# Kernel tuning notes

Measured on AMD Instinct MI355X. Metric: run time of the kernel, lower is better.

Reference implementation:

```python
import jax, jax.numpy as jnp
import numpy as np

N = 50000          # nodes
DEG = 8            # per-node in/out degree
E = N * DEG        # fwd edges (rev = reversed fwd)
H = 128            # hidden_dim
T = 4              # towers
F = H // T         # per-tower F_in (divide_input=True)
FO = H // T        # per-tower F_out
L = 2              # num_layers
IN_DIM = 128
OUT_DIM = 32
AVG_LOG = float(np.log(DEG + 1.0))  # avg of log(deg+1) from deg histogram (all deg==8)
BN_EPS = 1e-5
STD_EPS = 1e-5


def setup_inputs() -> dict:
    key = jax.random.key(0)
    ks = jax.random.split(key, 10)
    x = jax.random.normal(ks[0], (N, IN_DIM), jnp.float32)
    # every node appears exactly DEG times as dst and as src -> deg histogram delta at 8
    dst = jnp.repeat(jnp.arange(N, dtype=jnp.int32), DEG)
    src = jax.random.permutation(ks[1], dst)
    edge_fwd = jnp.stack([src, dst])  # [2, E]

    def rn(k, shape):
        return jax.random.normal(k, shape, jnp.float32) * 0.05

    return dict(
        x=x,
        W_in=rn(ks[2], (IN_DIM, H)), b_in=jnp.zeros((H,), jnp.float32),
        # [layer, relation(fwd/rev), tower, ...]
        pre_W=rn(ks[3], (L, 2, T, 2 * F, F)), pre_b=jnp.zeros((L, 2, T, F), jnp.float32),
        post_W=rn(ks[4], (L, 2, T, 13 * F, FO)), post_b=jnp.zeros((L, 2, T, FO), jnp.float32),
        lin_W=rn(ks[5], (L, 2, H, H)), lin_b=jnp.zeros((L, 2, H), jnp.float32),
        bn_gamma=jnp.ones((L, H), jnp.float32), bn_beta=jnp.zeros((L, H), jnp.float32),
        mlp_W1=rn(ks[6], (H, H)), mlp_b1=jnp.zeros((H,), jnp.float32),
        mlp_W2=rn(ks[7], (H, OUT_DIM)), mlp_b2=jnp.zeros((OUT_DIM,), jnp.float32),
        edge_fwd=edge_fwd,
    )


def _pna(x, src, dst, pre_W, pre_b, post_W, post_b, lin_W, lin_b):
    """One PNAConv (divide_input=True, pre/post_layers=1, no edge attr)."""
    xt = x.reshape(N, T, F)                                   # [N,T,F]
    # message: cat([x_i (dst), x_j (src)]) -> per-tower pre-MLP
    h = jnp.concatenate([xt[dst], xt[src]], axis=-1)          # [E,T,2F]
    m = jnp.einsum('etf,tfg->etg', h, pre_W) + pre_b          # [E,T,F]
    # multi-aggregator scatter reduce over destination nodes
    deg = jax.ops.segment_sum(jnp.ones((m.shape[0],), x.dtype), dst, N)
    degc = jnp.maximum(deg, 1.0)
    inv = (1.0 / degc)[:, None, None]
    mean = jax.ops.segment_sum(m, dst, N) * inv
    mean2 = jax.ops.segment_sum(m * m, dst, N) * inv
    std = jnp.sqrt(jax.nn.relu(mean2 - mean * mean) + STD_EPS)
    mn = jax.ops.segment_min(m, dst, N)
    mx = jax.ops.segment_max(m, dst, N)
    agg = jnp.concatenate([mean, mn, mx, std], axis=-1)       # [N,T,4F]
    # degree scalers: amplification, attenuation, identity
    ld = jnp.log(degc + 1.0)[:, None, None]
    agg = jnp.concatenate([agg * (ld / AVG_LOG), agg * (AVG_LOG / ld), agg], axis=-1)  # [N,T,12F]
    out = jnp.concatenate([xt, agg], axis=-1)                 # [N,T,13F]
    out = jnp.einsum('ntf,tfg->ntg', out, post_W) + post_b    # [N,T,FO]
    out = out.reshape(N, T * FO)
    return out @ lin_W + lin_b                                # [N,H]


def _bn(x, g, b):
    mu = x.mean(0)
    var = x.var(0)  # biased, as torch BatchNorm normalization
    return g * (x - mu) * jax.lax.rsqrt(var + BN_EPS) + b


def reference(x, W_in, b_in, pre_W, pre_b, post_W, post_b, lin_W, lin_b,
              bn_gamma, bn_beta, mlp_W1, mlp_b1, mlp_W2, mlp_b2, edge_fwd):
    src, dst = edge_fwd[0], edge_fwd[1]
    h = jax.nn.relu(x @ W_in + b_in)
    for l in range(L):
        # HeteroConv sum of fwd relation and rev relation (reversed edges)
        y = (_pna(h, src, dst, pre_W[l, 0], pre_b[l, 0], post_W[l, 0], post_b[l, 0], lin_W[l, 0], lin_b[l, 0])
             + _pna(h, dst, src, pre_W[l, 1], pre_b[l, 1], post_W[l, 1], post_b[l, 1], lin_W[l, 1], lin_b[l, 1]))
        h = jax.nn.relu(_bn(y, bn_gamma[l], bn_beta[l]))
        # dropout omitted (deterministic reference / eval mode)
    return jax.nn.relu(h @ mlp_W1 + mlp_b1) @ mlp_W2 + mlp_b2
```

## Files before the change

kernel.cpp:

```cpp
#include <hip/hip_runtime.h>
#include <hip/hip_fp16.h>
#include <cstddef>
#include <cstdint>

#define NN 50000
#define DEG 8
#define EE (NN*DEG)
#define RT_CNT 3125
#define KSTEPS 36
#define W8L 18432
#define MPAD 136

typedef __attribute__((ext_vector_type(8))) short short8;
typedef __attribute__((ext_vector_type(4))) float f32x4;

union Pack8 { __half h[8]; __half2 h2[4]; uint4 u; };
union Pack4 { __half h[4]; uint2 u; };

__global__ void k_build_nbr(const int* __restrict__ ef, int* __restrict__ cnt,
                            int* __restrict__ fwd_nbr, int* __restrict__ rev_nbr) {
    int e = blockIdx.x * blockDim.x + threadIdx.x;
    if (e >= EE) return;
    int s = ef[e], d = ef[EE + e];
    int p = atomicAdd(&cnt[d], 1);
    fwd_nbr[d * DEG + p] = s;
    int q = atomicAdd(&cnt[NN + s], 1);
    rev_nbr[s * DEG + q] = d;
}

__global__ __launch_bounds__(256) void k_wprep(
    const float* __restrict__ post_W, const float* __restrict__ pre_W,
    const float* __restrict__ pre_b, const float* __restrict__ post_b,
    const float* __restrict__ lin_W, const float* __restrict__ lin_b,
    __half* __restrict__ Wcp, float* __restrict__ Qw, float* __restrict__ bc) {
    __shared__ float Pf[160 * 33];
    __shared__ float Wl[32 * 128];
    __shared__ float Wt[32 * 32];
    __shared__ float Ps[32 * 32];
    __shared__ float Q[32 * 32];
    __shared__ float T3s[32];
    int tid = threadIdx.x;
    int m4 = blockIdx.x;
    int l = m4 >> 3, r = (m4 >> 2) & 1, tw = m4 & 3;
    const float* PW = post_W + (size_t)m4 * 416 * 32;
    for (int i = tid; i < 160 * 32; i += 256) {
        int row = i >> 5, g = i & 31;
        float v;
        if (row < 32) v = PW[row * 32 + g];
        else {
            int rr = row - 32;
            v = PW[(32 + rr) * 32 + g] + PW[(160 + rr) * 32 + g] + PW[(288 + rr) * 32 + g];
        }
        Pf[row * 33 + g] = v;
    }
    for (int i = tid; i < 1024; i += 256) Wt[i] = pre_W[(size_t)m4 * 2048 + i];
    for (int i = tid; i < 4096; i += 256)
        Wl[i] = lin_W[(size_t)(l * 2 + r) * 16384 + tw * 32 * 128 + i];
    __syncthreads();
    for (int i = tid; i < 1024; i += 256) {
        int g = i >> 5, j = i & 31;
        Ps[i] = Pf[(32 + g) * 33 + j] + Pf[(64 + g) * 33 + j] + Pf[(96 + g) * 33 + j];
    }
    __syncthreads();
    for (int i = tid; i < 1024; i += 256) {
        int f = i >> 5, j = i & 31;
        float acc = Pf[f * 33 + j];
#pragma unroll
        for (int g = 0; g < 32; g++) acc += Wt[f * 32 + g] * Ps[g * 32 + j];
        Q[i] = acc;
    }
    if (tid < 32) {
        int j = tid;
        float v = post_b[m4 * 32 + j];
#pragma unroll
        for (int g = 0; g < 32; g++) v += pre_b[m4 * 32 + g] * Ps[g * 32 + j];
        T3s[j] = v;
    }
    __syncthreads();
    for (int u = tid; u < 2048; u += 256) {
        int lane = u & 63, t = (u >> 6) & 7, s = u >> 9;
        int quad = lane >> 4, nl = lane & 15;
        int n = t * 16 + nl;
        Pack8 pk;
#pragma unroll
        for (int e = 0; e < 8; e++) {
            int f = quad * 8 + e;
            const float* Pr = &Pf[((s + 1) * 32 + f) * 33];
            float acc = 0.f;
#pragma unroll
            for (int j = 0; j < 32; j++) acc += Pr[j] * Wl[j * 128 + n];
            pk.h[e] = __float2half(acc);
        }
        int ks = 4 + r * 16 + tw * 4 + s;
        *(uint4*)&Wcp[((size_t)l * W8L + (t * KSTEPS + ks) * 64 + lane) * 8] = pk.u;
    }
    for (int i = tid; i < 4096; i += 256) {
        int f = i >> 7, n = i & 127;
        float acc = 0.f;
#pragma unroll
        for (int j = 0; j < 32; j++) acc += Q[f * 32 + j] * Wl[j * 128 + n];
        atomicAdd(&Qw[(size_t)l * 16384 + (tw * 32 + f) * 128 + n], acc);
    }
    if (tid < 128) {
        float v = 0.f;
#pragma unroll
        for (int j = 0; j < 32; j++) v += T3s[j] * Wl[j * 128 + tid];
        atomicAdd(&bc[l * 128 + tid], v);
        if ((m4 & 7) == 0)
            atomicAdd(&bc[l * 128 + tid],
                      lin_b[(2 * l) * 128 + tid] + lin_b[(2 * l + 1) * 128 + tid]);
    }
}

__global__ void k_pack_xt(const float* __restrict__ Qw, __half* __restrict__ Wcp) {
    int gid = blockIdx.x * blockDim.x + threadIdx.x;
    if (gid >= 2 * 4 * 8 * 64) return;
    int lane = gid & 63, t = (gid >> 6) & 7, ks = (gid >> 9) & 3, l = gid >> 11;
    int quad = lane >> 4;
    int n = t * 16 + (lane & 15);
    Pack8 pk;
#pragma unroll
    for (int e = 0; e < 8; e++)
        pk.h[e] = __float2half(Qw[(size_t)l * 16384 + (ks * 32 + quad * 8 + e) * 128 + n]);
    *(uint4*)&Wcp[((size_t)l * W8L + (t * KSTEPS + ks) * 64 + lane) * 8] = pk.u;
}

__global__ void k_pack_b(const float* __restrict__ W, int K, int N,
                         __half* __restrict__ dst) {
    int gid = blockIdx.x * blockDim.x + threadIdx.x;
    int total = (K >> 5) * (N >> 4) * 64;
    if (gid >= total) return;
    int lane = gid & 63;
    int ks = (gid >> 6) % (K >> 5);
    int t = (gid >> 6) / (K >> 5);
    int quad = lane >> 4, nl = lane & 15;
    int n = t * 16 + nl;
    Pack8 pk;
#pragma unroll
    for (int e = 0; e < 8; e++)
        pk.h[e] = __float2half(W[(size_t)(ks * 32 + quad * 8 + e) * N + n]);
    *(uint4*)&dst[(size_t)gid * 8] = pk.u;
}

__global__ __launch_bounds__(256) void k_in_mfma(
    const float* __restrict__ X, const __half* __restrict__ Wp,
    const float* __restrict__ b, float* __restrict__ H) {
    __shared__ __half Sh[4][16 * MPAD];
    int tid = threadIdx.x, wave = tid >> 6, lane = tid & 63;
    int rt = blockIdx.x * 4 + wave;
    if (rt >= RT_CNT) rt = RT_CNT - 1;
    __half* T = Sh[wave];
    const float4* X4 = (const float4*)X + (size_t)rt * 16 * 32;
#pragma unroll
    for (int i = 0; i < 8; i++) {
        int idx = i * 64 + lane;
        int row = idx >> 5, col4 = idx & 31;
        float4 v = X4[idx];
        Pack4 p4;
        p4.h[0] = __float2half(v.x); p4.h[1] = __float2half(v.y);
        p4.h[2] = __float2half(v.z); p4.h[3] = __float2half(v.w);
        *(uint2*)&T[row * MPAD + col4 * 4] = p4.u;
    }
    int mm = lane & 15, quad = lane >> 4;
    short8 a[4];
#pragma unroll
    for (int ks = 0; ks < 4; ks++)
        a[ks] = *(const short8*)&T[mm * MPAD + ks * 32 + quad * 8];
    const short8* Bb = (const short8*)Wp + lane;
    f32x4 acc[8];
#pragma unroll
    for (int t = 0; t < 8; t++) acc[t] = (f32x4){0.f, 0.f, 0.f, 0.f};
#pragma unroll
    for (int ks = 0; ks < 4; ks++)
#pragma unroll
        for (int t = 0; t < 8; t++)
            acc[t] = __builtin_amdgcn_mfma_f32_16x16x32_f16(
                a[ks], Bb[(t * 4 + ks) * 64], acc[t], 0, 0, 0);
#pragma unroll
    for (int t = 0; t < 8; t++) {
        int n = t * 16 + mm;
        float bias = b[n];
#pragma unroll
        for (int r = 0; r < 4; r++) {
            int node = rt * 16 + quad * 4 + r;
            H[(size_t)node * 128 + n] = fmaxf(acc[t][r] + bias, 0.f);
        }
    }
}

template<int BN>
__global__ __launch_bounds__(256) void k_preB(
    const float* __restrict__ Xin, const float* __restrict__ scale,
    const float* __restrict__ shift, float* __restrict__ hout,
    const float* __restrict__ pre_W, int layer, __half* __restrict__ Bplanes) {
    __shared__ float Wb[2 * 4 * 32 * 32];
    __shared__ float Xs[16 * 128];
    int tid = threadIdx.x;
    for (int i = tid; i < 8192; i += 256) {
        int g = i & 31, f = (i >> 5) & 31, t = (i >> 10) & 3, r = i >> 12;
        Wb[i] = pre_W[((((layer * 2 + r) * 4 + t) * 64) + 32 + f) * 32 + g];
    }
    int r = tid >> 7, c = tid & 127, t = c >> 5, g = c & 31;
    const float* wp = &Wb[((r * 4 + t) * 32) * 32 + g];
    int base = blockIdx.x * 16;
    for (int i = tid; i < 16 * 128; i += 256) {
        int col = i & 127;
        size_t gi = (size_t)(base + (i >> 7)) * 128 + col;
        float v = Xin[gi];
        if (BN) {
            v = fmaxf(scale[col] * v + shift[col], 0.f);
            hout[gi] = v;
        }
        Xs[i] = v;
    }
    __syncthreads();
    for (int n = 0; n < 16; n++) {
        float acc = 0.f;
#pragma unroll
        for (int f = 0; f < 32; f++) acc += Xs[n * 128 + t * 32 + f] * wp[f * 32];
        Bplanes[(size_t)r * NN * 128 + (size_t)(base + n) * 128 + c] = __float2half(acc);
    }
}

__global__ __launch_bounds__(256, 4) void k_agg_gemm(
    const float* __restrict__ hbuf, const __half* __restrict__ Bplanes,
    const int* __restrict__ fwd_nbr, const int* __restrict__ rev_nbr,
    const __half* __restrict__ Wcp, const float* __restrict__ bc,
    float* __restrict__ Y, float* __restrict__ bnsum, float* __restrict__ bnsum2) {
    __shared__ __half Spack[KSTEPS * 64 * 8];
    __shared__ float bnred[256];
    int tid = threadIdx.x;
    int blk = blockIdx.x;
    bnred[tid] = 0.f;
    int lane = tid & 63, wv = tid >> 6;
    int s = lane >> 4, f16 = lane & 15;
    int tw = f16 >> 2, quad = f16 & 3;
    int m = wv * 4 + s;
    int d = blk * 16 + m;
    {
        const int4* nf = (const int4*)&fwd_nbr[d * 8];
        const int4* nr = (const int4*)&rev_nbr[d * 8];
        int4 a0 = nf[0], a1 = nf[1], b0v = nr[0], b1v = nr[1];
        int idx0[8] = {a0.x, a0.y, a0.z, a0.w, a1.x, a1.y, a1.z, a1.w};
        int idx1[8] = {b0v.x, b0v.y, b0v.z, b0v.w, b1v.x, b1v.y, b1v.z, b1v.w};
        int fo = f16 * 8;
        Pack8 r0[8], r1[8];
        const __half* Bp1 = Bplanes + (size_t)NN * 128;
#pragma unroll
        for (int k = 0; k < 8; k++)
            r0[k].u = *(const uint4*)&Bplanes[(size_t)idx0[k] * 128 + fo];
#pragma unroll
        for (int k = 0; k < 8; k++)
            r1[k].u = *(const uint4*)&Bp1[(size_t)idx1[k] * 128 + fo];
        const float* Hp = &hbuf[(size_t)(blk * 16 + f16) * 128 + wv * 32 + s * 8];
        float4 xv0 = *(const float4*)Hp;
        float4 xv1 = *(const float4*)(Hp + 4);
        int pos = 16 * quad + (m ^ quad ^ ((tw & 1) << 2));
#pragma unroll
        for (int rel = 0; rel < 2; rel++) {
            Pack8* rr = rel ? r1 : r0;
            float sS[8], qS[8], mnS[8], mxS[8];
#pragma unroll
            for (int j = 0; j < 8; j++) {
                sS[j] = 0.f; qS[j] = 0.f; mnS[j] = 1e30f; mxS[j] = -1e30f;
            }
#pragma unroll
            for (int k = 0; k < 8; k++) {
#pragma unroll
                for (int j2 = 0; j2 < 4; j2++) {
                    __half2 h = rr[k].h2[j2];
                    float a = __half2float(__low2half(h));
                    float b = __half2float(__high2half(h));
                    int j0 = 2 * j2, j1 = j0 + 1;
                    sS[j0] += a; qS[j0] += a * a;
                    mnS[j0] = fminf(mnS[j0], a); mxS[j0] = fmaxf(mxS[j0], a);
                    sS[j1] += b; qS[j1] += b * b;
                    mnS[j1] = fminf(mnS[j1], b); mxS[j1] = fmaxf(mxS[j1], b);
                }
            }
            Pack8 mean, stdv, mnp, mxp;
#pragma unroll
            for (int j = 0; j < 8; j++) {
                float Bm = sS[j] * 0.125f;
                mean.h[j] = __float2half(Bm);
                stdv.h[j] = __float2half(
                    sqrtf(fmaxf(qS[j] * 0.125f - Bm * Bm, 0.f) + 1e-5f));
                mnp.h[j] = __float2half(mnS[j]);
                mxp.h[j] = __float2half(mxS[j]);
            }
            int ksb = 4 + rel * 16 + tw * 4;
            *(uint4*)&Spack[((size_t)(ksb + 0) * 64 + pos) * 8] = mean.u;
            *(uint4*)&Spack[((size_t)(ksb + 1) * 64 + pos) * 8] = mnp.u;
            *(uint4*)&Spack[((size_t)(ksb + 2) * 64 + pos) * 8] = mxp.u;
            *(uint4*)&Spack[((size_t)(ksb + 3) * 64 + pos) * 8] = stdv.u;
        }
        int posx = 16 * s + (f16 ^ s ^ ((wv & 1) << 2));
        Pack8 pk;
        pk.h[0] = __float2half(xv0.x); pk.h[1] = __float2half(xv0.y);
        pk.h[2] = __float2half(xv0.z); pk.h[3] = __float2half(xv0.w);
        pk.h[4] = __float2half(xv1.x); pk.h[5] = __float2half(xv1.y);
        pk.h[6] = __float2half(xv1.z); pk.h[7] = __float2half(xv1.w);
        *(uint4*)&Spack[((size_t)wv * 64 + posx) * 8] = pk.u;
    }
    __syncthreads();
    int mB = lane & 15, qB = lane >> 4;
    int t0 = wv * 2;
    const short8* Bb = (const short8*)Wcp + lane;
    f32x4 acc0 = (f32x4){0.f, 0.f, 0.f, 0.f};
    f32x4 acc1 = (f32x4){0.f, 0.f, 0.f, 0.f};
    short8 p0[6], p1[6];
#pragma unroll
    for (int dd = 0; dd < 6; dd++) {
        p0[dd] = Bb[((size_t)t0 * KSTEPS + dd) * 64];
        p1[dd] = Bb[((size_t)(t0 + 1) * KSTEPS + dd) * 64];
    }
#pragma unroll
    for (int ks = 0; ks < KSTEPS; ks++) {
        int twk = (ks < 4) ? ks : (((ks - 4) >> 2) & 3);
        int pos = 16 * qB + (mB ^ qB ^ ((twk & 1) << 2));
        short8 a = *(const short8*)&Spack[((size_t)ks * 64 + pos) * 8];
        acc0 = __builtin_amdgcn_mfma_f32_16x16x32_f16(a, p0[ks % 6], acc0, 0, 0, 0);
        acc1 = __builtin_amdgcn_mfma_f32_16x16x32_f16(a, p1[ks % 6], acc1, 0, 0, 0);
        if (ks + 6 < KSTEPS) {
            p0[ks % 6] = Bb[((size_t)t0 * KSTEPS + ks + 6) * 64];
            p1[ks % 6] = Bb[((size_t)(t0 + 1) * KSTEPS + ks + 6) * 64];
        }
    }
    int nl = lane & 15, qd = lane >> 4;
#pragma unroll
    for (int tt = 0; tt < 2; tt++) {
        f32x4 acc = tt ? acc1 : acc0;
        int n = (t0 + tt) * 16 + nl;
        float bias = bc[n];
        float ls = 0.f, ls2 = 0.f;
#pragma unroll
        for (int r = 0; r < 4; r++) {
            float v = acc[r] + bias;
            int node = blk * 16 + qd * 4 + r;
            Y[(size_t)node * 128 + n] = v;
            ls += v; ls2 += v * v;
        }
        ls += __shfl_xor(ls, 16); ls += __shfl_xor(ls, 32);
        ls2 += __shfl_xor(ls2, 16); ls2 += __shfl_xor(ls2, 32);
        if (qd == 0) { bnred[n] += ls; bnred[128 + n] += ls2; }
    }
    __syncthreads();
    if (tid < 128) {
        atomicAdd(&bnsum[tid], bnred[tid]);
        atomicAdd(&bnsum2[tid], bnred[128 + tid]);
    }
}

__global__ void k_bn_final(const float* __restrict__ bnsum, const float* __restrict__ bnsum2,
                           const float* __restrict__ gamma, const float* __restrict__ beta,
                           int layer, float* __restrict__ scale, float* __restrict__ shift) {
    int c = threadIdx.x;
    float mu = bnsum[c] * (1.f / NN);
    float var = bnsum2[c] * (1.f / NN) - mu * mu;
    float sc = gamma[layer * 128 + c] * rsqrtf(var + 1e-5f);
    scale[c] = sc;
    shift[c] = beta[layer * 128 + c] - mu * sc;
}

__global__ __launch_bounds__(256) void k_mlp_mfma(
    const float* __restrict__ Yb, const float* __restrict__ scale,
    const float* __restrict__ shift, const __half* __restrict__ W1p,
    const float* __restrict__ b1, const __half* __restrict__ W2p,
    const float* __restrict__ b2, float* __restrict__ out) {
    __shared__ __half Sh[4][16 * MPAD];
    int tid = threadIdx.x, wave = tid >> 6, lane = tid & 63;
    int rt = blockIdx.x * 4 + wave;
    if (rt >= RT_CNT) rt = RT_CNT - 1;
    __half* T = Sh[wave];
    const float4* Y4 = (const float4*)Yb + (size_t)rt * 16 * 32;
    const float4* sc4 = (const float4*)scale;
    const float4* sh4 = (const float4*)shift;
#pragma unroll
    for (int i = 0; i < 8; i++) {
        int idx = i * 64 + lane;
        int row = idx >> 5, col4 = idx & 31;
        float4 v = Y4[idx];
        float4 s = sc4[col4], f = sh4[col4];
        Pack4 p4;
        p4.h[0] = __float2half(fmaxf(s.x * v.x + f.x, 0.f));
        p4.h[1] = __float2half(fmaxf(s.y * v.y + f.y, 0.f));
        p4.h[2] = __float2half(fmaxf(s.z * v.z + f.z, 0.f));
        p4.h[3] = __float2half(fmaxf(s.w * v.w + f.w, 0.f));
        *(uint2*)&T[row * MPAD + col4 * 4] = p4.u;
    }
    int mm = lane & 15, quad = lane >> 4;
    short8 a[4];
#pragma unroll
    for (int ks = 0; ks < 4; ks++)
        a[ks] = *(const short8*)&T[mm * MPAD + ks * 32 + quad * 8];
    const short8* B1 = (const short8*)W1p + lane;
    f32x4 acc[8];
#pragma unroll
    for (int t = 0; t < 8; t++) acc[t] = (f32x4){0.f, 0.f, 0.f, 0.f};
#pragma unroll
    for (int ks = 0; ks < 4; ks++)
#pragma unroll
        for (int t = 0; t < 8; t++)
            acc[t] = __builtin_amdgcn_mfma_f32_16x16x32_f16(
                a[ks], B1[(t * 4 + ks) * 64], acc[t], 0, 0, 0);
#pragma unroll
    for (int t = 0; t < 8; t++) {
        int n = t * 16 + mm;
        float bias = b1[n];
#pragma unroll
        for (int r = 0; r < 4; r++)
            T[(quad * 4 + r) * MPAD + n] = __float2half(fmaxf(acc[t][r] + bias, 0.f));
    }
    short8 a2[4];
#pragma unroll
    for (int ks = 0; ks < 4; ks++)
        a2[ks] = *(const short8*)&T[mm * MPAD + ks * 32 + quad * 8];
    const short8* B2 = (const short8*)W2p + lane;
    f32x4 acc2[2];
#pragma unroll
    for (int t = 0; t < 2; t++) acc2[t] = (f32x4){0.f, 0.f, 0.f, 0.f};
#pragma unroll
    for (int ks = 0; ks < 4; ks++)
#pragma unroll
        for (int t = 0; t < 2; t++)
            acc2[t] = __builtin_amdgcn_mfma_f32_16x16x32_f16(
                a2[ks], B2[(t * 4 + ks) * 64], acc2[t], 0, 0, 0);
#pragma unroll
    for (int t = 0; t < 2; t++) {
        int n = t * 16 + mm;
        float bias = b2[n];
#pragma unroll
        for (int r = 0; r < 4; r++)
            out[(size_t)(rt * 16 + quad * 4 + r) * 32 + n] = acc2[t][r] + bias;
    }
}

extern "C" void kernel_launch(void* const* d_in, const int* in_sizes, int n_in,
                              void* d_out, int out_size, void* d_ws, size_t ws_size,
                              hipStream_t stream) {
    const float* x      = (const float*)d_in[0];
    const float* W_in   = (const float*)d_in[1];
    const float* b_in   = (const float*)d_in[2];
    const float* pre_W  = (const float*)d_in[3];
    const float* pre_b  = (const float*)d_in[4];
    const float* post_W = (const float*)d_in[5];
    const float* post_b = (const float*)d_in[6];
    const float* lin_W  = (const float*)d_in[7];
    const float* lin_b  = (const float*)d_in[8];
    const float* bn_g   = (const float*)d_in[9];
    const float* bn_b   = (const float*)d_in[10];
    const float* mlp_W1 = (const float*)d_in[11];
    const float* mlp_b1 = (const float*)d_in[12];
    const float* mlp_W2 = (const float*)d_in[13];
    const float* mlp_b2 = (const float*)d_in[14];
    const int*   edge   = (const int*)d_in[15];
    float* out = (float*)d_out;

    char* w = (char*)d_ws;
    const size_t plane = (size_t)NN * 128 * sizeof(float);
    float* hbuf = (float*)w; w += plane;
    float* ybuf = (float*)w; w += plane;
    __half* Bpl = (__half*)w; w += plane;
    int* fwd_nbr = (int*)w; w += (size_t)NN * DEG * sizeof(int);
    int* rev_nbr = (int*)w; w += (size_t)NN * DEG * sizeof(int);
    int* cnt     = (int*)w; w += (size_t)2 * NN * sizeof(int);
    float* Qw    = (float*)w; w += (size_t)2 * 128 * 128 * sizeof(float);
    float* bc    = (float*)w; w += 2 * 128 * sizeof(float);
    __half* Wcp  = (__half*)w; w += (size_t)2 * KSTEPS * 32 * 128 * sizeof(__half);
    __half* Winp = (__half*)w; w += (size_t)128 * 128 * sizeof(__half);
    __half* W1p  = (__half*)w; w += (size_t)128 * 128 * sizeof(__half);
    __half* W2p  = (__half*)w; w += (size_t)128 * 32 * sizeof(__half);
    float* bnsum  = (float*)w; w += 128 * sizeof(float);
    float* bnsum2 = (float*)w; w += 128 * sizeof(float);
    float* scale  = (float*)w; w += 128 * sizeof(float);
    float* shift  = (float*)w; w += 128 * sizeof(float);

    const int gWave = (RT_CNT + 3) / 4;

    (void)hipMemsetAsync(cnt, 0, (size_t)2 * NN * sizeof(int), stream);
    (void)hipMemsetAsync(Qw, 0, (size_t)(2 * 128 * 128 + 2 * 128) * sizeof(float), stream);
    k_build_nbr<<<(EE + 255) / 256, 256, 0, stream>>>(edge, cnt, fwd_nbr, rev_nbr);
    k_wprep<<<16, 256, 0, stream>>>(post_W, pre_W, pre_b, post_b, lin_W, lin_b,
                                    Wcp, Qw, bc);
    k_pack_xt<<<16, 256, 0, stream>>>(Qw, Wcp);
    k_pack_b<<<8, 256, 0, stream>>>(W_in, 128, 128, Winp);
    k_pack_b<<<8, 256, 0, stream>>>(mlp_W1, 128, 128, W1p);
    k_pack_b<<<2, 256, 0, stream>>>(mlp_W2, 128, 32, W2p);

    k_in_mfma<<<gWave, 256, 0, stream>>>(x, Winp, b_in, hbuf);

    for (int l = 0; l < 2; l++) {
        if (l == 0)
            k_preB<0><<<RT_CNT, 256, 0, stream>>>(hbuf, nullptr, nullptr, nullptr,
                                                  pre_W, 0, Bpl);
        else
            k_preB<1><<<RT_CNT, 256, 0, stream>>>(ybuf, scale, shift, hbuf,
                                                  pre_W, 1, Bpl);
        (void)hipMemsetAsync(bnsum, 0, 2 * 128 * sizeof(float), stream);
        k_agg_gemm<<<RT_CNT, 256, 0, stream>>>(
            hbuf, Bpl, fwd_nbr, rev_nbr, Wcp + (size_t)l * KSTEPS * 32 * 128,
            bc + l * 128, ybuf, bnsum, bnsum2);
        k_bn_final<<<1, 128, 0, stream>>>(bnsum, bnsum2, bn_g, bn_b, l, scale, shift);
    }

    k_mlp_mfma<<<gWave, 256, 0, stream>>>(ybuf, scale, shift, W1p, mlp_b1,
                                          W2p, mlp_b2, out);
}
```

Measured before the change: 458.3 us.

## Store hidden state in fp16 and software-pipeline gathers across tiles in agg kernel

The hidden-state buffer is now stored as fp16 instead of fp32, which halves its write and read traffic in the input, preB and aggregation kernels. The aggregation kernel now processes four row tiles per block and issues the neighbor gathers for the next tile while the MFMA GEMM of the current tile runs. This also cuts the number of block-level BN atomics. The costs are higher register pressure from the prefetched gather buffers (the occupancy hint was dropped), fewer blocks to spread across CUs, and extra rounding of the hidden state.

```diff
diff --git a/kernel.cpp b/kernel.cpp
--- a/kernel.cpp
+++ b/kernel.cpp
@@ -10,6 +10,7 @@
 #define KSTEPS 36
 #define W8L 18432
 #define MPAD 136
+#define TPB 4
 
 typedef __attribute__((ext_vector_type(8))) short short8;
 typedef __attribute__((ext_vector_type(4))) float f32x4;
@@ -144,7 +145,7 @@
 
 __global__ __launch_bounds__(256) void k_in_mfma(
     const float* __restrict__ X, const __half* __restrict__ Wp,
-    const float* __restrict__ b, float* __restrict__ H) {
+    const float* __restrict__ b, __half* __restrict__ H) {
     __shared__ __half Sh[4][16 * MPAD];
     int tid = threadIdx.x, wave = tid >> 6, lane = tid & 63;
     int rt = blockIdx.x * 4 + wave;
@@ -183,16 +184,17 @@
 #pragma unroll
         for (int r = 0; r < 4; r++) {
             int node = rt * 16 + quad * 4 + r;
-            H[(size_t)node * 128 + n] = fmaxf(acc[t][r] + bias, 0.f);
+            H[(size_t)node * 128 + n] = __float2half(fmaxf(acc[t][r] + bias, 0.f));
         }
     }
 }
 
 template<int BN>
 __global__ __launch_bounds__(256) void k_preB(
-    const float* __restrict__ Xin, const float* __restrict__ scale,
-    const float* __restrict__ shift, float* __restrict__ hout,
-    const float* __restrict__ pre_W, int layer, __half* __restrict__ Bplanes) {
+    const __half* __restrict__ Xh, const float* __restrict__ Xf,
+    const float* __restrict__ scale, const float* __restrict__ shift,
+    __half* __restrict__ hout, const float* __restrict__ pre_W,
+    int layer, __half* __restrict__ Bplanes) {
     __shared__ float Wb[2 * 4 * 32 * 32];
     __shared__ float Xs[16 * 128];
     int tid = threadIdx.x;
@@ -206,10 +208,12 @@
     for (int i = tid; i < 16 * 128; i += 256) {
         int col = i & 127;
         size_t gi = (size_t)(base + (i >> 7)) * 128 + col;
-        float v = Xin[gi];
+        float v;
         if (BN) {
-            v = fmaxf(scale[col] * v + shift[col], 0.f);
-            hout[gi] = v;
+            v = fmaxf(scale[col] * Xf[gi] + shift[col], 0.f);
+            hout[gi] = __float2half(v);
+        } else {
+            v = __half2float(Xh[gi]);
         }
         Xs[i] = v;
     }
@@ -222,43 +226,55 @@
     }
 }
 
-__global__ __launch_bounds__(256, 4) void k_agg_gemm(
-    const float* __restrict__ hbuf, const __half* __restrict__ Bplanes,
+__global__ __launch_bounds__(256) void k_agg_gemm(
+    const __half* __restrict__ hbuf, const __half* __restrict__ Bplanes,
     const int* __restrict__ fwd_nbr, const int* __restrict__ rev_nbr,
     const __half* __restrict__ Wcp, const float* __restrict__ bc,
     float* __restrict__ Y, float* __restrict__ bnsum, float* __restrict__ bnsum2) {
     __shared__ __half Spack[KSTEPS * 64 * 8];
     __shared__ float bnred[256];
     int tid = threadIdx.x;
-    int blk = blockIdx.x;
     bnred[tid] = 0.f;
     int lane = tid & 63, wv = tid >> 6;
     int s = lane >> 4, f16 = lane & 15;
     int tw = f16 >> 2, quad = f16 & 3;
     int m = wv * 4 + s;
-    int d = blk * 16 + m;
-    {
+    int fo = f16 * 8;
+    int pos = 16 * quad + (m ^ quad ^ ((tw & 1) << 2));
+    int posx = 16 * s + (f16 ^ s ^ ((wv & 1) << 2));
+    const __half* Bp1 = Bplanes + (size_t)NN * 128;
+    int tbase = blockIdx.x * TPB;
+
+    Pack8 raw0[8], raw1[8], xraw;
+    auto issue = [&](int rt) {
+        int rtc = rt < RT_CNT ? rt : RT_CNT - 1;
+        int d = rtc * 16 + m;
         const int4* nf = (const int4*)&fwd_nbr[d * 8];
         const int4* nr = (const int4*)&rev_nbr[d * 8];
-        int4 a0 = nf[0], a1 = nf[1], b0v = nr[0], b1v = nr[1];
-        int idx0[8] = {a0.x, a0.y, a0.z, a0.w, a1.x, a1.y, a1.z, a1.w};
-        int idx1[8] = {b0v.x, b0v.y, b0v.z, b0v.w, b1v.x, b1v.y, b1v.z, b1v.w};
-        int fo = f16 * 8;
-        Pack8 r0[8], r1[8];
-        const __half* Bp1 = Bplanes + (size_t)NN * 128;
+        int4 a0 = nf[0], a1 = nf[1], c0 = nr[0], c1 = nr[1];
+        int i0[8] = {a0.x, a0.y, a0.z, a0.w, a1.x, a1.y, a1.z, a1.w};
+        int i1[8] = {c0.x, c0.y, c0.z, c0.w, c1.x, c1.y, c1.z, c1.w};
 #pragma unroll
         for (int k = 0; k < 8; k++)
-            r0[k].u = *(const uint4*)&Bplanes[(size_t)idx0[k] * 128 + fo];
+            raw0[k].u = *(const uint4*)&Bplanes[(size_t)i0[k] * 128 + fo];
 #pragma unroll
         for (int k = 0; k < 8; k++)
-            r1[k].u = *(const uint4*)&Bp1[(size_t)idx1[k] * 128 + fo];
-        const float* Hp = &hbuf[(size_t)(blk * 16 + f16) * 128 + wv * 32 + s * 8];
-        float4 xv0 = *(const float4*)Hp;
-        float4 xv1 = *(const float4*)(Hp + 4);
-        int pos = 16 * quad + (m ^ quad ^ ((tw & 1) << 2));
+            raw1[k].u = *(const uint4*)&Bp1[(size_t)i1[k] * 128 + fo];
+        xraw.u = *(const uint4*)&hbuf[(size_t)(rtc * 16 + f16) * 128 + wv * 32 + s * 8];
+    };
+
+    issue(tbase);
+    int mB = lane & 15, qB = lane >> 4;
+    int t0 = wv * 2;
+    const short8* Bb = (const short8*)Wcp + lane;
+
+#pragma unroll
+    for (int i = 0; i < TPB; i++) {
+        int rt = tbase + i;
+        bool valid = rt < RT_CNT;
 #pragma unroll
         for (int rel = 0; rel < 2; rel++) {
-            Pack8* rr = rel ? r1 : r0;
+            Pack8* rr = rel ? raw1 : raw0;
             float sS[8], qS[8], mnS[8], mxS[8];
 #pragma unroll
             for (int j = 0; j < 8; j++) {
@@ -294,57 +310,50 @@
             *(uint4*)&Spack[((size_t)(ksb + 2) * 64 + pos) * 8] = mxp.u;
             *(uint4*)&Spack[((size_t)(ksb + 3) * 64 + pos) * 8] = stdv.u;
         }
-        int posx = 16 * s + (f16 ^ s ^ ((wv & 1) << 2));
-        Pack8 pk;
-        pk.h[0] = __float2half(xv0.x); pk.h[1] = __float2half(xv0.y);
-        pk.h[2] = __float2half(xv0.z); pk.h[3] = __float2half(xv0.w);
-        pk.h[4] = __float2half(xv1.x); pk.h[5] = __float2half(xv1.y);
-        pk.h[6] = __float2half(xv1.z); pk.h[7] = __float2half(xv1.w);
-        *(uint4*)&Spack[((size_t)wv * 64 + posx) * 8] = pk.u;
-    }
-    __syncthreads();
-    int mB = lane & 15, qB = lane >> 4;
-    int t0 = wv * 2;
-    const short8* Bb = (const short8*)Wcp + lane;
-    f32x4 acc0 = (f32x4){0.f, 0.f, 0.f, 0.f};
-    f32x4 acc1 = (f32x4){0.f, 0.f, 0.f, 0.f};
-    short8 p0[6], p1[6];
-#pragma unroll
-    for (int dd = 0; dd < 6; dd++) {
-        p0[dd] = Bb[((size_t)t0 * KSTEPS + dd) * 64];
-        p1[dd] = Bb[((size_t)(t0 + 1) * KSTEPS + dd) * 64];
-    }
-#pragma unroll
-    for (int ks = 0; ks < KSTEPS; ks++) {
-        int twk = (ks < 4) ? ks : (((ks - 4) >> 2) & 3);
-        int pos = 16 * qB + (mB ^ qB ^ ((twk & 1) << 2));
-        short8 a = *(const short8*)&Spack[((size_t)ks * 64 + pos) * 8];
-        acc0 = __builtin_amdgcn_mfma_f32_16x16x32_f16(a, p0[ks % 6], acc0, 0, 0, 0);
-        acc1 = __builtin_amdgcn_mfma_f32_16x16x32_f16(a, p1[ks % 6], acc1, 0, 0, 0);
-        if (ks + 6 < KSTEPS) {
-            p0[ks % 6] = Bb[((size_t)t0 * KSTEPS + ks + 6) * 64];
-            p1[ks % 6] = Bb[((size_t)(t0 + 1) * KSTEPS + ks + 6) * 64];
-        }
-    }
-    int nl = lane & 15, qd = lane >> 4;
-#pragma unroll
-    for (int tt = 0; tt < 2; tt++) {
-        f32x4 acc = tt ? acc1 : acc0;
-        int n = (t0 + tt) * 16 + nl;
-        float bias = bc[n];
-        float ls = 0.f, ls2 = 0.f;
-#pragma unroll
-        for (int r = 0; r < 4; r++) {
-            float v = acc[r] + bias;
-            int node = blk * 16 + qd * 4 + r;
-            Y[(size_t)node * 128 + n] = v;
-            ls += v; ls2 += v * v;
-        }
-        ls += __shfl_xor(ls, 16); ls += __shfl_xor(ls, 32);
-        ls2 += __shfl_xor(ls2, 16); ls2 += __shfl_xor(ls2, 32);
-        if (qd == 0) { bnred[n] += ls; bnred[128 + n] += ls2; }
-    }
-    __syncthreads();
+        *(uint4*)&Spack[((size_t)wv * 64 + posx) * 8] = xraw.u;
+        __syncthreads();
+        if (i + 1 < TPB) issue(rt + 1);
+        f32x4 acc0 = (f32x4){0.f, 0.f, 0.f, 0.f};
+        f32x4 acc1 = (f32x4){0.f, 0.f, 0.f, 0.f};
+        short8 p0[6], p1[6];
+#pragma unroll
+        for (int dd = 0; dd < 6; dd++) {
+            p0[dd] = Bb[((size_t)t0 * KSTEPS + dd) * 64];
+            p1[dd] = Bb[((size_t)(t0 + 1) * KSTEPS + dd) * 64];
+        }
+#pragma unroll
+        for (int ks = 0; ks < KSTEPS; ks++) {
+            int twk = (ks < 4) ? ks : (((ks - 4) >> 2) & 3);
+            int posr = 16 * qB + (mB ^ qB ^ ((twk & 1) << 2));
+            short8 a = *(const short8*)&Spack[((size_t)ks * 64 + posr) * 8];
+            acc0 = __builtin_amdgcn_mfma_f32_16x16x32_f16(a, p0[ks % 6], acc0, 0, 0, 0);
+            acc1 = __builtin_amdgcn_mfma_f32_16x16x32_f16(a, p1[ks % 6], acc1, 0, 0, 0);
+            if (ks + 6 < KSTEPS) {
+                p0[ks % 6] = Bb[((size_t)t0 * KSTEPS + ks + 6) * 64];
+                p1[ks % 6] = Bb[((size_t)(t0 + 1) * KSTEPS + ks + 6) * 64];
+            }
+        }
+        if (valid) {
+#pragma unroll
+            for (int tt = 0; tt < 2; tt++) {
+                f32x4 acc = tt ? acc1 : acc0;
+                int n = (t0 + tt) * 16 + mB;
+                float bias = bc[n];
+                float ls = 0.f, ls2 = 0.f;
+#pragma unroll
+                for (int r = 0; r < 4; r++) {
+                    float v = acc[r] + bias;
+                    int node = rt * 16 + qB * 4 + r;
+                    Y[(size_t)node * 128 + n] = v;
+                    ls += v; ls2 += v * v;
+                }
+                ls += __shfl_xor(ls, 16); ls += __shfl_xor(ls, 32);
+                ls2 += __shfl_xor(ls2, 16); ls2 += __shfl_xor(ls2, 32);
+                if (qB == 0) { bnred[n] += ls; bnred[128 + n] += ls2; }
+            }
+        }
+        __syncthreads();
+    }
     if (tid < 128) {
         atomicAdd(&bnsum[tid], bnred[tid]);
         atomicAdd(&bnsum2[tid], bnred[128 + tid]);
@@ -458,7 +467,7 @@
 
     char* w = (char*)d_ws;
     const size_t plane = (size_t)NN * 128 * sizeof(float);
-    float* hbuf = (float*)w; w += plane;
+    __half* hbuf = (__half*)w; w += plane / 2;
     float* ybuf = (float*)w; w += plane;
     __half* Bpl = (__half*)w; w += plane;
     int* fwd_nbr = (int*)w; w += (size_t)NN * DEG * sizeof(int);
@@ -476,6 +485,7 @@
     float* shift  = (float*)w; w += 128 * sizeof(float);
 
     const int gWave = (RT_CNT + 3) / 4;
+    const int gAgg  = (RT_CNT + TPB - 1) / TPB;
 
     (void)hipMemsetAsync(cnt, 0, (size_t)2 * NN * sizeof(int), stream);
     (void)hipMemsetAsync(Qw, 0, (size_t)(2 * 128 * 128 + 2 * 128) * sizeof(float), stream);
@@ -492,12 +502,12 @@
     for (int l = 0; l < 2; l++) {
         if (l == 0)
             k_preB<0><<<RT_CNT, 256, 0, stream>>>(hbuf, nullptr, nullptr, nullptr,
-                                                  pre_W, 0, Bpl);
+                                                  nullptr, pre_W, 0, Bpl);
         else
-            k_preB<1><<<RT_CNT, 256, 0, stream>>>(ybuf, scale, shift, hbuf,
-                                                  pre_W, 1, Bpl);
+            k_preB<1><<<RT_CNT, 256, 0, stream>>>(nullptr, ybuf, scale, shift,
+                                                  hbuf, pre_W, 1, Bpl);
         (void)hipMemsetAsync(bnsum, 0, 2 * 128 * sizeof(float), stream);
-        k_agg_gemm<<<RT_CNT, 256, 0, stream>>>(
+        k_agg_gemm<<<gAgg, 256, 0, stream>>>(
             hbuf, Bpl, fwd_nbr, rev_nbr, Wcp + (size_t)l * KSTEPS * 32 * 128,
             bc + l * 128, ybuf, bnsum, bnsum2);
         k_bn_final<<<1, 128, 0, stream>>>(bnsum, bnsum2, bn_g, bn_b, l, scale, shift);
```

Measured after the change: 496.6 us. +8.3%, slower.

## Move pre-MLP projection to MFMA, store hidden state in fp16, fold BN finalize

Applied to the files above, without the earlier changes.

Replaces the scalar fp32 pre-transform kernel with an MFMA kernel that uses a block-diagonal packed fp16 weight, one launch per layer covering both relations. The hidden state buffer becomes fp16, written through LDS as coalesced 16-byte stores, which halves its traffic in the aggregation kernel. The BatchNorm scale/shift computation is folded into the consuming kernels, which removes the k_bn_final launches and per-layer memsets. MFMA A-operands are now loaded straight from global memory instead of staged through LDS, and the LDS row pad shrinks. The block-diagonal weight does four times the useful FLOPs, and fp16 storage of h reduces precision.

```diff
diff --git a/kernel.cpp b/kernel.cpp
--- a/kernel.cpp
+++ b/kernel.cpp
@@ -9,13 +9,12 @@
 #define RT_CNT 3125
 #define KSTEPS 36
 #define W8L 18432
-#define MPAD 136
+#define MPAD 132
 
 typedef __attribute__((ext_vector_type(8))) short short8;
 typedef __attribute__((ext_vector_type(4))) float f32x4;
 
-union Pack8 { __half h[8]; __half2 h2[4]; uint4 u; };
-union Pack4 { __half h[4]; uint2 u; };
+union Pack8 { __half h[8]; __half2 h2[4]; uint4 u; short8 s8; };
 
 __global__ void k_build_nbr(const int* __restrict__ ef, int* __restrict__ cnt,
                             int* __restrict__ fwd_nbr, int* __restrict__ rev_nbr) {
@@ -142,30 +141,46 @@
     *(uint4*)&dst[(size_t)gid * 8] = pk.u;
 }
 
+__global__ void k_pack_wbd(const float* __restrict__ pre_W, __half* __restrict__ dst) {
+    int gid = blockIdx.x * blockDim.x + threadIdx.x;
+    if (gid >= 2 * 2 * 8 * 4 * 64) return;
+    int lane = gid & 63, ks = (gid >> 6) & 3, t8 = (gid >> 8) & 7;
+    int rel = (gid >> 11) & 1, l = gid >> 12;
+    int quad = lane >> 4, nl = lane & 15;
+    int n = t8 * 16 + nl;
+    int tn = n >> 5;
+    Pack8 pk;
+#pragma unroll
+    for (int e = 0; e < 8; e++) {
+        int k = ks * 32 + quad * 8 + e;
+        float v = 0.f;
+        if ((k >> 5) == tn)
+            v = pre_W[(size_t)((((l * 2 + rel) * 4 + tn) * 64) + 32 + (k & 31)) * 32 + (n & 31)];
+        pk.h[e] = __float2half(v);
+    }
+    *(uint4*)&dst[((size_t)(l * 2 + rel) * 2048 + (t8 * 4 + ks) * 64 + lane) * 8] = pk.u;
+}
+
 __global__ __launch_bounds__(256) void k_in_mfma(
     const float* __restrict__ X, const __half* __restrict__ Wp,
-    const float* __restrict__ b, float* __restrict__ H) {
+    const float* __restrict__ b, __half* __restrict__ H) {
     __shared__ __half Sh[4][16 * MPAD];
-    int tid = threadIdx.x, wave = tid >> 6, lane = tid & 63;
-    int rt = blockIdx.x * 4 + wave;
+    int tid = threadIdx.x, wv = tid >> 6, lane = tid & 63;
+    int rt = blockIdx.x * 4 + wv;
     if (rt >= RT_CNT) rt = RT_CNT - 1;
-    __half* T = Sh[wave];
-    const float4* X4 = (const float4*)X + (size_t)rt * 16 * 32;
-#pragma unroll
-    for (int i = 0; i < 8; i++) {
-        int idx = i * 64 + lane;
-        int row = idx >> 5, col4 = idx & 31;
-        float4 v = X4[idx];
-        Pack4 p4;
-        p4.h[0] = __float2half(v.x); p4.h[1] = __float2half(v.y);
-        p4.h[2] = __float2half(v.z); p4.h[3] = __float2half(v.w);
-        *(uint2*)&T[row * MPAD + col4 * 4] = p4.u;
-    }
     int mm = lane & 15, quad = lane >> 4;
     short8 a[4];
 #pragma unroll
-    for (int ks = 0; ks < 4; ks++)
-        a[ks] = *(const short8*)&T[mm * MPAD + ks * 32 + quad * 8];
+    for (int ks = 0; ks < 4; ks++) {
+        const float4* p = (const float4*)&X[(size_t)(rt * 16 + mm) * 128 + ks * 32 + quad * 8];
+        float4 v0 = p[0], v1 = p[1];
+        Pack8 pk;
+        pk.h[0] = __float2half(v0.x); pk.h[1] = __float2half(v0.y);
+        pk.h[2] = __float2half(v0.z); pk.h[3] = __float2half(v0.w);
+        pk.h[4] = __float2half(v1.x); pk.h[5] = __float2half(v1.y);
+        pk.h[6] = __float2half(v1.z); pk.h[7] = __float2half(v1.w);
+        a[ks] = pk.s8;
+    }
     const short8* Bb = (const short8*)Wp + lane;
     f32x4 acc[8];
 #pragma unroll
@@ -176,54 +191,104 @@
         for (int t = 0; t < 8; t++)
             acc[t] = __builtin_amdgcn_mfma_f32_16x16x32_f16(
                 a[ks], Bb[(t * 4 + ks) * 64], acc[t], 0, 0, 0);
+    __half* T = Sh[wv];
 #pragma unroll
     for (int t = 0; t < 8; t++) {
         int n = t * 16 + mm;
         float bias = b[n];
 #pragma unroll
-        for (int r = 0; r < 4; r++) {
-            int node = rt * 16 + quad * 4 + r;
-            H[(size_t)node * 128 + n] = fmaxf(acc[t][r] + bias, 0.f);
-        }
-    }
-}
-
-template<int BN>
-__global__ __launch_bounds__(256) void k_preB(
-    const float* __restrict__ Xin, const float* __restrict__ scale,
-    const float* __restrict__ shift, float* __restrict__ hout,
-    const float* __restrict__ pre_W, int layer, __half* __restrict__ Bplanes) {
-    __shared__ float Wb[2 * 4 * 32 * 32];
-    __shared__ float Xs[16 * 128];
-    int tid = threadIdx.x;
-    for (int i = tid; i < 8192; i += 256) {
-        int g = i & 31, f = (i >> 5) & 31, t = (i >> 10) & 3, r = i >> 12;
-        Wb[i] = pre_W[((((layer * 2 + r) * 4 + t) * 64) + 32 + f) * 32 + g];
-    }
-    int r = tid >> 7, c = tid & 127, t = c >> 5, g = c & 31;
-    const float* wp = &Wb[((r * 4 + t) * 32) * 32 + g];
-    int base = blockIdx.x * 16;
-    for (int i = tid; i < 16 * 128; i += 256) {
-        int col = i & 127;
-        size_t gi = (size_t)(base + (i >> 7)) * 128 + col;
-        float v = Xin[gi];
-        if (BN) {
-            v = fmaxf(scale[col] * v + shift[col], 0.f);
-            hout[gi] = v;
-        }
-        Xs[i] = v;
-    }
-    __syncthreads();
-    for (int n = 0; n < 16; n++) {
-        float acc = 0.f;
-#pragma unroll
-        for (int f = 0; f < 32; f++) acc += Xs[n * 128 + t * 32 + f] * wp[f * 32];
-        Bplanes[(size_t)r * NN * 128 + (size_t)(base + n) * 128 + c] = __float2half(acc);
+        for (int r = 0; r < 4; r++)
+            T[(quad * 4 + r) * MPAD + n] = __float2half(fmaxf(acc[t][r] + bias, 0.f));
+    }
+#pragma unroll
+    for (int it = 0; it < 4; it++) {
+        int idx = it * 64 + lane;
+        int row = idx >> 4, col = (idx & 15) * 8;
+        *(uint4*)&H[(size_t)(rt * 16 + row) * 128 + col] = *(uint4*)&T[row * MPAD + col];
+    }
+}
+
+template<int V>
+__global__ __launch_bounds__(256) void k_preB_mfma(
+    const __half* __restrict__ Hin, const float* __restrict__ Yf,
+    const float* __restrict__ bns, const float* __restrict__ bns2,
+    const float* __restrict__ gamma, const float* __restrict__ beta,
+    __half* __restrict__ Hout, const __half* __restrict__ WbBDp,
+    __half* __restrict__ Bplanes) {
+    __shared__ __half Sh[4][16 * MPAD];
+    __shared__ float sc[128], sh[128];
+    int tid = threadIdx.x, wv = tid >> 6, lane = tid & 63;
+    int rt = blockIdx.x * 4 + wv;
+    if (rt >= RT_CNT) rt = RT_CNT - 1;
+    if (V == 2) {
+        if (tid < 128) {
+            float mu = bns[tid] * (1.f / NN);
+            float var = bns2[tid] * (1.f / NN) - mu * mu;
+            float s = gamma[tid] * rsqrtf(var + 1e-5f);
+            sc[tid] = s;
+            sh[tid] = beta[tid] - mu * s;
+        }
+        __syncthreads();
+    }
+    int mm = lane & 15, quad = lane >> 4;
+    short8 a[4];
+#pragma unroll
+    for (int ks = 0; ks < 4; ks++) {
+        int c0 = ks * 32 + quad * 8;
+        size_t base = (size_t)(rt * 16 + mm) * 128 + c0;
+        if (V == 1) {
+            Pack8 pk; pk.u = *(const uint4*)&Hin[base];
+            a[ks] = pk.s8;
+        } else {
+            const float4* p = (const float4*)&Yf[base];
+            float4 v0 = p[0], v1 = p[1];
+            float4 s0 = *(const float4*)&sc[c0], s1 = *(const float4*)&sc[c0 + 4];
+            float4 f0 = *(const float4*)&sh[c0], f1 = *(const float4*)&sh[c0 + 4];
+            Pack8 pk;
+            pk.h[0] = __float2half(fmaxf(s0.x * v0.x + f0.x, 0.f));
+            pk.h[1] = __float2half(fmaxf(s0.y * v0.y + f0.y, 0.f));
+            pk.h[2] = __float2half(fmaxf(s0.z * v0.z + f0.z, 0.f));
+            pk.h[3] = __float2half(fmaxf(s0.w * v0.w + f0.w, 0.f));
+            pk.h[4] = __float2half(fmaxf(s1.x * v1.x + f1.x, 0.f));
+            pk.h[5] = __float2half(fmaxf(s1.y * v1.y + f1.y, 0.f));
+            pk.h[6] = __float2half(fmaxf(s1.z * v1.z + f1.z, 0.f));
+            pk.h[7] = __float2half(fmaxf(s1.w * v1.w + f1.w, 0.f));
+            *(uint4*)&Hout[base] = pk.u;
+            a[ks] = pk.s8;
+        }
+    }
+    __half* T = Sh[wv];
+#pragma unroll
+    for (int rel = 0; rel < 2; rel++) {
+        const short8* Bb = (const short8*)WbBDp + (size_t)rel * 2048 + lane;
+        f32x4 acc[8];
+#pragma unroll
+        for (int t = 0; t < 8; t++) acc[t] = (f32x4){0.f, 0.f, 0.f, 0.f};
+#pragma unroll
+        for (int ks = 0; ks < 4; ks++)
+#pragma unroll
+            for (int t = 0; t < 8; t++)
+                acc[t] = __builtin_amdgcn_mfma_f32_16x16x32_f16(
+                    a[ks], Bb[(t * 4 + ks) * 64], acc[t], 0, 0, 0);
+#pragma unroll
+        for (int t = 0; t < 8; t++) {
+            int n = t * 16 + mm;
+#pragma unroll
+            for (int r = 0; r < 4; r++)
+                T[(quad * 4 + r) * MPAD + n] = __float2half(acc[t][r]);
+        }
+        __half* Bp = Bplanes + (size_t)rel * NN * 128;
+#pragma unroll
+        for (int it = 0; it < 4; it++) {
+            int idx = it * 64 + lane;
+            int row = idx >> 4, col = (idx & 15) * 8;
+            *(uint4*)&Bp[(size_t)(rt * 16 + row) * 128 + col] = *(uint4*)&T[row * MPAD + col];
+        }
     }
 }
 
 __global__ __launch_bounds__(256, 4) void k_agg_gemm(
-    const float* __restrict__ hbuf, const __half* __restrict__ Bplanes,
+    const __half* __restrict__ hbuf, const __half* __restrict__ Bplanes,
     const int* __restrict__ fwd_nbr, const int* __restrict__ rev_nbr,
     const __half* __restrict__ Wcp, const float* __restrict__ bc,
     float* __restrict__ Y, float* __restrict__ bnsum, float* __restrict__ bnsum2) {
@@ -252,9 +317,8 @@
 #pragma unroll
         for (int k = 0; k < 8; k++)
             r1[k].u = *(const uint4*)&Bp1[(size_t)idx1[k] * 128 + fo];
-        const float* Hp = &hbuf[(size_t)(blk * 16 + f16) * 128 + wv * 32 + s * 8];
-        float4 xv0 = *(const float4*)Hp;
-        float4 xv1 = *(const float4*)(Hp + 4);
+        Pack8 xr;
+        xr.u = *(const uint4*)&hbuf[(size_t)(blk * 16 + f16) * 128 + wv * 32 + s * 8];
         int pos = 16 * quad + (m ^ quad ^ ((tw & 1) << 2));
 #pragma unroll
         for (int rel = 0; rel < 2; rel++) {
@@ -295,12 +359,7 @@
             *(uint4*)&Spack[((size_t)(ksb + 3) * 64 + pos) * 8] = stdv.u;
         }
         int posx = 16 * s + (f16 ^ s ^ ((wv & 1) << 2));
-        Pack8 pk;
-        pk.h[0] = __float2half(xv0.x); pk.h[1] = __float2half(xv0.y);
-        pk.h[2] = __float2half(xv0.z); pk.h[3] = __float2half(xv0.w);
-        pk.h[4] = __float2half(xv1.x); pk.h[5] = __float2half(xv1.y);
-        pk.h[6] = __float2half(xv1.z); pk.h[7] = __float2half(xv1.w);
-        *(uint4*)&Spack[((size_t)wv * 64 + posx) * 8] = pk.u;
+        *(uint4*)&Spack[((size_t)wv * 64 + posx) * 8] = xr.u;
     }
     __syncthreads();
     int mB = lane & 15, qB = lane >> 4;
@@ -317,8 +376,8 @@
 #pragma unroll
     for (int ks = 0; ks < KSTEPS; ks++) {
         int twk = (ks < 4) ? ks : (((ks - 4) >> 2) & 3);
-        int pos = 16 * qB + (mB ^ qB ^ ((twk & 1) << 2));
-        short8 a = *(const short8*)&Spack[((size_t)ks * 64 + pos) * 8];
+        int posr = 16 * qB + (mB ^ qB ^ ((twk & 1) << 2));
+        short8 a = *(const short8*)&Spack[((size_t)ks * 64 + posr) * 8];
         acc0 = __builtin_amdgcn_mfma_f32_16x16x32_f16(a, p0[ks % 6], acc0, 0, 0, 0);
         acc1 = __builtin_amdgcn_mfma_f32_16x16x32_f16(a, p1[ks % 6], acc1, 0, 0, 0);
         if (ks + 6 < KSTEPS) {
@@ -326,23 +385,22 @@
             p1[ks % 6] = Bb[((size_t)(t0 + 1) * KSTEPS + ks + 6) * 64];
         }
     }
-    int nl = lane & 15, qd = lane >> 4;
 #pragma unroll
     for (int tt = 0; tt < 2; tt++) {
         f32x4 acc = tt ? acc1 : acc0;
-        int n = (t0 + tt) * 16 + nl;
+        int n = (t0 + tt) * 16 + mB;
         float bias = bc[n];
         float ls = 0.f, ls2 = 0.f;
 #pragma unroll
         for (int r = 0; r < 4; r++) {
             float v = acc[r] + bias;
-            int node = blk * 16 + qd * 4 + r;
+            int node = blk * 16 + qB * 4 + r;
             Y[(size_t)node * 128 + n] = v;
             ls += v; ls2 += v * v;
         }
         ls += __shfl_xor(ls, 16); ls += __shfl_xor(ls, 32);
         ls2 += __shfl_xor(ls2, 16); ls2 += __shfl_xor(ls2, 32);
-        if (qd == 0) { bnred[n] += ls; bnred[128 + n] += ls2; }
+        if (qB == 0) { bnred[n] += ls; bnred[128 + n] += ls2; }
     }
     __syncthreads();
     if (tid < 128) {
@@ -351,48 +409,45 @@
     }
 }
 
-__global__ void k_bn_final(const float* __restrict__ bnsum, const float* __restrict__ bnsum2,
-                           const float* __restrict__ gamma, const float* __restrict__ beta,
-                           int layer, float* __restrict__ scale, float* __restrict__ shift) {
-    int c = threadIdx.x;
-    float mu = bnsum[c] * (1.f / NN);
-    float var = bnsum2[c] * (1.f / NN) - mu * mu;
-    float sc = gamma[layer * 128 + c] * rsqrtf(var + 1e-5f);
-    scale[c] = sc;
-    shift[c] = beta[layer * 128 + c] - mu * sc;
-}
-
 __global__ __launch_bounds__(256) void k_mlp_mfma(
-    const float* __restrict__ Yb, const float* __restrict__ scale,
-    const float* __restrict__ shift, const __half* __restrict__ W1p,
+    const float* __restrict__ Yb, const float* __restrict__ bns,
+    const float* __restrict__ bns2, const float* __restrict__ gamma,
+    const float* __restrict__ beta, const __half* __restrict__ W1p,
     const float* __restrict__ b1, const __half* __restrict__ W2p,
     const float* __restrict__ b2, float* __restrict__ out) {
     __shared__ __half Sh[4][16 * MPAD];
-    int tid = threadIdx.x, wave = tid >> 6, lane = tid & 63;
-    int rt = blockIdx.x * 4 + wave;
+    __shared__ float sc[128], sh[128];
+    int tid = threadIdx.x, wv = tid >> 6, lane = tid & 63;
+    int rt = blockIdx.x * 4 + wv;
     if (rt >= RT_CNT) rt = RT_CNT - 1;
-    __half* T = Sh[wave];
-    const float4* Y4 = (const float4*)Yb + (size_t)rt * 16 * 32;
-    const float4* sc4 = (const float4*)scale;
-    const float4* sh4 = (const float4*)shift;
-#pragma unroll
-    for (int i = 0; i < 8; i++) {
-        int idx = i * 64 + lane;
-        int row = idx >> 5, col4 = idx & 31;
-        float4 v = Y4[idx];
-        float4 s = sc4[col4], f = sh4[col4];
-        Pack4 p4;
-        p4.h[0] = __float2half(fmaxf(s.x * v.x + f.x, 0.f));
-        p4.h[1] = __float2half(fmaxf(s.y * v.y + f.y, 0.f));
-        p4.h[2] = __float2half(fmaxf(s.z * v.z + f.z, 0.f));
-        p4.h[3] = __float2half(fmaxf(s.w * v.w + f.w, 0.f));
-        *(uint2*)&T[row * MPAD + col4 * 4] = p4.u;
-    }
+    if (tid < 128) {
+        float mu = bns[tid] * (1.f / NN);
+        float var = bns2[tid] * (1.f / NN) - mu * mu;
+        float s = gamma[tid] * rsqrtf(var + 1e-5f);
+        sc[tid] = s;
+        sh[tid] = beta[tid] - mu * s;
+    }
+    __syncthreads();
     int mm = lane & 15, quad = lane >> 4;
     short8 a[4];
 #pragma unroll
-    for (int ks = 0; ks < 4; ks++)
-        a[ks] = *(const short8*)&T[mm * MPAD + ks * 32 + quad * 8];
+    for (int ks = 0; ks < 4; ks++) {
+        int c0 = ks * 32 + quad * 8;
+        const float4* p = (const float4*)&Yb[(size_t)(rt * 16 + mm) * 128 + c0];
+        float4 v0 = p[0], v1 = p[1];
+        float4 s0 = *(const float4*)&sc[c0], s1 = *(const float4*)&sc[c0 + 4];
+        float4 f0 = *(const float4*)&sh[c0], f1 = *(const float4*)&sh[c0 + 4];
+        Pack8 pk;
+        pk.h[0] = __float2half(fmaxf(s0.x * v0.x + f0.x, 0.f));
+        pk.h[1] = __float2half(fmaxf(s0.y * v0.y + f0.y, 0.f));
+        pk.h[2] = __float2half(fmaxf(s0.z * v0.z + f0.z, 0.f));
+        pk.h[3] = __float2half(fmaxf(s0.w * v0.w + f0.w, 0.f));
+        pk.h[4] = __float2half(fmaxf(s1.x * v1.x + f1.x, 0.f));
+        pk.h[5] = __float2half(fmaxf(s1.y * v1.y + f1.y, 0.f));
+        pk.h[6] = __float2half(fmaxf(s1.z * v1.z + f1.z, 0.f));
+        pk.h[7] = __float2half(fmaxf(s1.w * v1.w + f1.w, 0.f));
+        a[ks] = pk.s8;
+    }
     const short8* B1 = (const short8*)W1p + lane;
     f32x4 acc[8];
 #pragma unroll
@@ -403,6 +458,7 @@
         for (int t = 0; t < 8; t++)
             acc[t] = __builtin_amdgcn_mfma_f32_16x16x32_f16(
                 a[ks], B1[(t * 4 + ks) * 64], acc[t], 0, 0, 0);
+    __half* T = Sh[wv];
 #pragma unroll
     for (int t = 0; t < 8; t++) {
         int n = t * 16 + mm;
@@ -458,7 +514,7 @@
 
     char* w = (char*)d_ws;
     const size_t plane = (size_t)NN * 128 * sizeof(float);
-    float* hbuf = (float*)w; w += plane;
+    __half* hbuf = (__half*)w; w += plane / 2;
     float* ybuf = (float*)w; w += plane;
     __half* Bpl = (__half*)w; w += plane;
     int* fwd_nbr = (int*)w; w += (size_t)NN * DEG * sizeof(int);
@@ -470,15 +526,14 @@
     __half* Winp = (__half*)w; w += (size_t)128 * 128 * sizeof(__half);
     __half* W1p  = (__half*)w; w += (size_t)128 * 128 * sizeof(__half);
     __half* W2p  = (__half*)w; w += (size_t)128 * 32 * sizeof(__half);
-    float* bnsum  = (float*)w; w += 128 * sizeof(float);
-    float* bnsum2 = (float*)w; w += 128 * sizeof(float);
-    float* scale  = (float*)w; w += 128 * sizeof(float);
-    float* shift  = (float*)w; w += 128 * sizeof(float);
+    __half* WbBD = (__half*)w; w += (size_t)4 * 128 * 128 * sizeof(__half);
+    float* bns   = (float*)w; w += 4 * 128 * sizeof(float);
 
     const int gWave = (RT_CNT + 3) / 4;
 
     (void)hipMemsetAsync(cnt, 0, (size_t)2 * NN * sizeof(int), stream);
     (void)hipMemsetAsync(Qw, 0, (size_t)(2 * 128 * 128 + 2 * 128) * sizeof(float), stream);
+    (void)hipMemsetAsync(bns, 0, 4 * 128 * sizeof(float), stream);
     k_build_nbr<<<(EE + 255) / 256, 256, 0, stream>>>(edge, cnt, fwd_nbr, rev_nbr);
     k_wprep<<<16, 256, 0, stream>>>(post_W, pre_W, pre_b, post_b, lin_W, lin_b,
                                     Wcp, Qw, bc);
@@ -486,23 +541,23 @@
     k_pack_b<<<8, 256, 0, stream>>>(W_in, 128, 128, Winp);
     k_pack_b<<<8, 256, 0, stream>>>(mlp_W1, 128, 128, W1p);
     k_pack_b<<<2, 256, 0, stream>>>(mlp_W2, 128, 32, W2p);
+    k_pack_wbd<<<32, 256, 0, stream>>>(pre_W, WbBD);
 
     k_in_mfma<<<gWave, 256, 0, stream>>>(x, Winp, b_in, hbuf);
 
-    for (int l = 0; l < 2; l++) {
-        if (l == 0)
-            k_preB<0><<<RT_CNT, 256, 0, stream>>>(hbuf, nullptr, nullptr, nullptr,
-                                                  pre_W, 0, Bpl);
-        else
-            k_preB<1><<<RT_CNT, 256, 0, stream>>>(ybuf, scale, shift, hbuf,
-                                                  pre_W, 1, Bpl);
-        (void)hipMemsetAsync(bnsum, 0, 2 * 128 * sizeof(float), stream);
-        k_agg_gemm<<<RT_CNT, 256, 0, stream>>>(
-            hbuf, Bpl, fwd_nbr, rev_nbr, Wcp + (size_t)l * KSTEPS * 32 * 128,
-            bc + l * 128, ybuf, bnsum, bnsum2);
-        k_bn_final<<<1, 128, 0, stream>>>(bnsum, bnsum2, bn_g, bn_b, l, scale, shift);
-    }
-
-    k_mlp_mfma<<<gWave, 256, 0, stream>>>(ybuf, scale, shift, W1p, mlp_b1,
-                                          W2p, mlp_b2, out);
-}
+    k_preB_mfma<1><<<gWave, 256, 0, stream>>>(
+        hbuf, nullptr, nullptr, nullptr, nullptr, nullptr, nullptr,
+        WbBD, Bpl);
+    k_agg_gemm<<<RT_CNT, 256, 0, stream>>>(
+        hbuf, Bpl, fwd_nbr, rev_nbr, Wcp, bc, ybuf, bns, bns + 128);
+    k_preB_mfma<2><<<gWave, 256, 0, stream>>>(
+        nullptr, ybuf, bns, bns + 128, bn_g, bn_b, hbuf,
+        WbBD + (size_t)2 * 128 * 128, Bpl);
+    k_agg_gemm<<<RT_CNT, 256, 0, stream>>>(
+        hbuf, Bpl, fwd_nbr, rev_nbr, Wcp + (size_t)KSTEPS * 32 * 128,
+        bc + 128, ybuf, bns + 256, bns + 384);
+
+    k_mlp_mfma<<<gWave, 256, 0, stream>>>(ybuf, bns + 256, bns + 384,
+                                          bn_g + 128, bn_b + 128,
+                                          W1p, mlp_b1, W2p, mlp_b2, out);
+}
```

After: 456.7 us. No clear change (-0.4%).
